# Kernel tuning notes

Measured on AMD Instinct MI355X. Metric: run time of the kernel, lower is better.

## Reference

```python
import jax, jax.numpy as jnp
import numpy as np

EMBED = 1024
HEADS = 16
HEAD_DIM = EMBED // HEADS
BATCH = 4
SEQ = 2048


def setup_inputs() -> dict:
    key = jax.random.key(0)
    ks = jax.random.split(key, 9)
    s = 1.0 / np.sqrt(EMBED)
    inp = {
        "x": jax.random.normal(ks[0], (BATCH, SEQ, EMBED), dtype=jnp.float32),
        "Wq": jax.random.normal(ks[1], (EMBED, EMBED), dtype=jnp.float32) * s,
        "bq": jnp.zeros((EMBED,), jnp.float32),
        "Wk": jax.random.normal(ks[2], (EMBED, EMBED), dtype=jnp.float32) * s,
        "bk": jnp.zeros((EMBED,), jnp.float32),
        "Wv": jax.random.normal(ks[3], (EMBED, EMBED), dtype=jnp.float32) * s,
        "bv": jnp.zeros((EMBED,), jnp.float32),
        "Wo": jax.random.normal(ks[4], (EMBED, EMBED), dtype=jnp.float32) * s,
        "bo": jnp.zeros((EMBED,), jnp.float32),
    }
    return inp


def reference(x, Wq, bq, Wk, bk, Wv, bv, Wo, bo):
    B, S, E = x.shape
    H, D = HEADS, HEAD_DIM
    # projections (torch Linear with weight stored as [in,out] here)
    q = (x @ Wq + bq).reshape(B, S, H, D).transpose(0, 2, 1, 3)  # [B,H,S,D]
    k = (x @ Wk + bk).reshape(B, S, H, D).transpose(0, 2, 1, 3)
    v = (x @ Wv + bv).reshape(B, S, H, D).transpose(0, 2, 1, 3)
    scores = jnp.einsum('bhqd,bhkd->bhqk', q, k) * (1.0 / np.sqrt(D))
    causal = jnp.tril(jnp.ones((S, S), dtype=bool))
    scores = jnp.where(causal[None, None], scores, -jnp.inf)
    attn = jax.nn.softmax(scores, axis=-1)  # dropout p=0.0 -> identity
    out = jnp.einsum('bhqk,bhkd->bhqd', attn, v)  # [B,H,S,D]
    out = out.transpose(0, 2, 1, 3).reshape(B, S, E)
    return out @ Wo + bo
```

## Files before the change

### kernel.cpp

```cpp
#include <hip/hip_runtime.h>
#include <stdint.h>

#define EMBED 1024
#define SEQ   2048
#define BATCH 4
#define HEADS 16
#define HDIM  64
#define LDP   72

typedef unsigned short ushort_t;
typedef __bf16 bf16x8 __attribute__((ext_vector_type(8)));
typedef __bf16 bf16x4 __attribute__((ext_vector_type(4)));
typedef float  f32x4  __attribute__((ext_vector_type(4)));
typedef float  f32x16 __attribute__((ext_vector_type(16)));

#define MFMA16 __builtin_amdgcn_mfma_f32_16x16x32_bf16
#define MFMA32 __builtin_amdgcn_mfma_f32_32x32x16_bf16

typedef __attribute__((address_space(3))) uint32_t lds_u32_t;
typedef __attribute__((address_space(1))) const uint32_t glb_u32_t;

__device__ __forceinline__ void gl_lds16(const ushort_t* g, ushort_t* l) {
    __builtin_amdgcn_global_load_lds((glb_u32_t*)g, (lds_u32_t*)l, 16, 0, 0);
}

__device__ __forceinline__ ushort_t f2bf(float f) {
    union { float f; uint32_t u; } c; c.f = f;
    uint32_t u = c.u;
    return (ushort_t)((u + 0x7FFFu + ((u >> 16) & 1u)) >> 16);
}

__device__ __forceinline__ float exp2f_fast(float x) {
    float r; asm("v_exp_f32 %0, %1" : "=v"(r) : "v"(x)); return r;
}

__global__ __launch_bounds__(256)
void cast_x(const float* __restrict__ X, ushort_t* __restrict__ Xb)
{
    size_t i = ((size_t)blockIdx.x * 256 + threadIdx.x) * 8;
    ushort_t tmp[8];
    #pragma unroll
    for (int e = 0; e < 8; ++e) tmp[e] = f2bf(X[i + e]);
    *(uint4*)(Xb + i) = *(const uint4*)tmp;
}

__global__ __launch_bounds__(256)
void cast_transpose_w(const float* __restrict__ W, ushort_t* __restrict__ Wt)
{
    __shared__ ushort_t Ts[64 * 80];
    const int t = threadIdx.x;
    const int k0 = blockIdx.x * 64, n0 = blockIdx.y * 64;
    const int r = t >> 2, cs = (t & 3) * 16;
    const float* src = W + (size_t)(k0 + r) * EMBED + n0 + cs;
    #pragma unroll
    for (int e = 0; e < 16; ++e) Ts[(cs + e) * 80 + r] = f2bf(src[e]);
    __syncthreads();
    const int n = t >> 2, ks = (t & 3) * 16;
    ushort_t* dst = Wt + (size_t)(n0 + n) * EMBED + k0 + ks;
    *(uint4*)(dst)     = *(const uint4*)(&Ts[n * 80 + ks]);
    *(uint4*)(dst + 8) = *(const uint4*)(&Ts[n * 80 + ks + 8]);
}

__global__ __launch_bounds__(256)
void gemm_qkv(const ushort_t* __restrict__ A, const ushort_t* __restrict__ Bt,
              const float* __restrict__ bq, const float* __restrict__ bk,
              const float* __restrict__ bv, ushort_t* __restrict__ Cq, size_t tsz)
{
    __shared__ ushort_t As[128 * 32];
    __shared__ ushort_t Bs[128 * 32];
    const int t = threadIdx.x;
    const int wave = t >> 6, lane = t & 63;
    const int l15 = lane & 15, quad = lane >> 4;
    const int m0 = blockIdx.y * 128, n0 = blockIdx.x * 128;
    const int wm = (wave >> 1) * 64, wn = (wave & 1) * 64;
    f32x4 acc[4][4] = {};

    const int srow = wave * 32 + (lane >> 2), scol = (lane & 3) * 8;
    const ushort_t* Ag = A  + (size_t)(m0 + srow) * EMBED + scol;
    const ushort_t* Bg = Bt + (size_t)(n0 + srow) * EMBED + scol;
    ushort_t* AsW = As + wave * 1024;
    ushort_t* BsW = Bs + wave * 1024;

    for (int k0 = 0; k0 < EMBED; k0 += 32) {
        gl_lds16(Ag + k0,              AsW);
        gl_lds16(Ag + k0 + 16 * EMBED, AsW + 512);
        gl_lds16(Bg + k0,              BsW);
        gl_lds16(Bg + k0 + 16 * EMBED, BsW + 512);
        __syncthreads();

        bf16x8 af[4], bfr[4];
        #pragma unroll
        for (int mt = 0; mt < 4; ++mt)
            af[mt] = *(const bf16x8*)(&As[(wm + mt * 16 + l15) * 32 + quad * 8]);
        #pragma unroll
        for (int nt = 0; nt < 4; ++nt)
            bfr[nt] = *(const bf16x8*)(&Bs[(wn + nt * 16 + l15) * 32 + quad * 8]);
        #pragma unroll
        for (int mt = 0; mt < 4; ++mt)
            #pragma unroll
            for (int nt = 0; nt < 4; ++nt)
                acc[mt][nt] = MFMA16(af[mt], bfr[nt], acc[mt][nt], 0, 0, 0);
        __syncthreads();
    }

    const int mat = blockIdx.x >> 3;
    const float* bias = (mat == 0) ? bq : (mat == 1) ? bk : bv;
    const float scale = (mat == 0) ? 0.18033688011112042f : 1.0f;
    ushort_t* C = Cq + (size_t)mat * tsz;
    const int nc0 = (blockIdx.x & 7) * 128;
    #pragma unroll
    for (int nt = 0; nt < 4; ++nt) {
        int col = nc0 + wn + nt * 16 + l15;
        float bb = bias[col];
        #pragma unroll
        for (int mt = 0; mt < 4; ++mt)
            #pragma unroll
            for (int r = 0; r < 4; ++r) {
                int row = m0 + wm + mt * 16 + quad * 4 + r;
                C[(size_t)row * EMBED + col] = f2bf((acc[mt][nt][r] + bb) * scale);
            }
    }
}

__global__ __launch_bounds__(256)
void gemm_o(const ushort_t* __restrict__ A, const ushort_t* __restrict__ Bt,
            const float* __restrict__ bias, float* __restrict__ C)
{
    __shared__ ushort_t As[128 * 32];
    __shared__ ushort_t Bs[128 * 32];
    const int t = threadIdx.x;
    const int wave = t >> 6, lane = t & 63;
    const int l15 = lane & 15, quad = lane >> 4;
    const int m0 = blockIdx.y * 128, n0 = blockIdx.x * 128;
    const int wm = (wave >> 1) * 64, wn = (wave & 1) * 64;
    f32x4 acc[4][4] = {};

    const int srow = wave * 32 + (lane >> 2), scol = (lane & 3) * 8;
    const ushort_t* Ag = A  + (size_t)(m0 + srow) * EMBED + scol;
    const ushort_t* Bg = Bt + (size_t)(n0 + srow) * EMBED + scol;
    ushort_t* AsW = As + wave * 1024;
    ushort_t* BsW = Bs + wave * 1024;

    for (int k0 = 0; k0 < EMBED; k0 += 32) {
        gl_lds16(Ag + k0,              AsW);
        gl_lds16(Ag + k0 + 16 * EMBED, AsW + 512);
        gl_lds16(Bg + k0,              BsW);
        gl_lds16(Bg + k0 + 16 * EMBED, BsW + 512);
        __syncthreads();

        bf16x8 af[4], bfr[4];
        #pragma unroll
        for (int mt = 0; mt < 4; ++mt)
            af[mt] = *(const bf16x8*)(&As[(wm + mt * 16 + l15) * 32 + quad * 8]);
        #pragma unroll
        for (int nt = 0; nt < 4; ++nt)
            bfr[nt] = *(const bf16x8*)(&Bs[(wn + nt * 16 + l15) * 32 + quad * 8]);
        #pragma unroll
        for (int mt = 0; mt < 4; ++mt)
            #pragma unroll
            for (int nt = 0; nt < 4; ++nt)
                acc[mt][nt] = MFMA16(af[mt], bfr[nt], acc[mt][nt], 0, 0, 0);
        __syncthreads();
    }

    #pragma unroll
    for (int nt = 0; nt < 4; ++nt) {
        int col = n0 + wn + nt * 16 + l15;
        float bb = bias[col];
        #pragma unroll
        for (int mt = 0; mt < 4; ++mt)
            #pragma unroll
            for (int r = 0; r < 4; ++r) {
                int row = m0 + wm + mt * 16 + quad * 4 + r;
                C[(size_t)row * EMBED + col] = acc[mt][nt][r] + bb;
            }
    }
}

__global__ __launch_bounds__(256)
void transpose_v(const ushort_t* __restrict__ V, ushort_t* __restrict__ Vt)
{
    int blk = blockIdx.x;
    int st = blk & 31, bh = blk >> 5;
    int h = bh & 15, b = bh >> 4;
    int s0 = st * 64;
    __shared__ ushort_t Ts[64 * LDP];
    int tid = threadIdx.x;
    int r = tid >> 2, g = (tid & 3) * 8;

    const ushort_t* src = V + ((size_t)(b * SEQ + s0 + r)) * EMBED + h * HDIM;
    uint4 v0 = *(const uint4*)(src + g);
    uint4 v1 = *(const uint4*)(src + g + 32);
    const ushort_t* e0 = (const ushort_t*)&v0;
    const ushort_t* e1 = (const ushort_t*)&v1;
    #pragma unroll
    for (int e = 0; e < 8; ++e) Ts[(g + e) * LDP + r] = e0[e];
    #pragma unroll
    for (int e = 0; e < 8; ++e) Ts[(g + 32 + e) * LDP + r] = e1[e];
    __syncthreads();

    int d = tid >> 2;
    ushort_t* dst = Vt + ((size_t)bh * HDIM + d) * SEQ + s0;
    *(uint4*)(dst + g)      = *(const uint4*)(&Ts[d * LDP + g]);
    *(uint4*)(dst + g + 32) = *(const uint4*)(&Ts[d * LDP + g + 32]);
}

__global__ __launch_bounds__(256)
void flash_attn(const ushort_t* __restrict__ Q, const ushort_t* __restrict__ K,
                const ushort_t* __restrict__ Vt, ushort_t* __restrict__ O)
{
    const int logical = (blockIdx.x & 7) * 128 + (blockIdx.x >> 3);
    const int bh = logical >> 4;
    const int pb = 15 - (logical & 15);
    const int h = bh & 15, b = bh >> 4;
    const int t = threadIdx.x, w = t >> 6, lane = t & 63;
    const int l31 = lane & 31, hi = lane >> 5;
    const int s = pb * 4 + w;
    const int sdiag = s >> 1;
    const int lastJt = 2 * pb + 1;
    const size_t qkbase = (size_t)b * SEQ * EMBED + (size_t)h * HDIM;
    const size_t vtbase = (size_t)bh * HDIM * SEQ;

    __shared__ ushort_t KsB[2][64 * 64];
    __shared__ ushort_t VsB[2][64 * 64];
    __shared__ float Ls[4][32];

    bf16x8 qb[4];
    const ushort_t* qrow = Q + qkbase + (size_t)(s * 32 + l31) * EMBED + hi * 8;
    #pragma unroll
    for (int ks = 0; ks < 4; ++ks)
        qb[ks] = *(const bf16x8*)(qrow + ks * 16);

    const int rr = lane >> 3, cc = lane & 7;
    const ushort_t* KgL = K  + qkbase + (size_t)(w * 16 + rr) * EMBED + ((cc ^ rr) * 8);
    const ushort_t* VgL = Vt + vtbase + (size_t)(w * 16 + rr) * SEQ  + ((cc ^ rr) * 8);

    f32x16 o0 = {}, o1 = {};
    float l_part = 0.f;

    {
        ushort_t* kd = &KsB[0][w * 1024];
        ushort_t* vd = &VsB[0][w * 1024];
        gl_lds16(KgL,             kd);
        gl_lds16(KgL + 8 * EMBED, kd + 512);
        gl_lds16(VgL,             vd);
        gl_lds16(VgL + 8 * SEQ,   vd + 512);
    }

    int cur = 0;
    for (int jt = 0; jt <= lastJt; ++jt) {
        __syncthreads();

        if (jt < lastJt) {
            const ushort_t* kg = KgL + (size_t)(jt + 1) * 64 * EMBED;
            const ushort_t* vg = VgL + (jt + 1) * 64;
            ushort_t* kd = &KsB[cur ^ 1][w * 1024];
            ushort_t* vd = &VsB[cur ^ 1][w * 1024];
            gl_lds16(kg,             kd);
            gl_lds16(kg + 8 * EMBED, kd + 512);
            gl_lds16(vg,             vd);
            gl_lds16(vg + 8 * SEQ,   vd + 512);
        }

        if (jt <= sdiag) {
            const ushort_t* Kst = &KsB[cur][0];
            const ushort_t* Vst = &VsB[cur][0];
            const bool dg = (jt == sdiag);
            const bool skip1 = dg && !(s & 1);
            const bool mask0 = dg && !(s & 1);
            const bool mask1 = dg && (s & 1);
            const int swz = l31 & 7;

            f32x16 st0 = {}, st1 = {};
            #pragma unroll
            for (int ks = 0; ks < 4; ++ks) {
                bf16x8 ka = *(const bf16x8*)(Kst + l31 * 64 + (((ks * 2 + hi) ^ swz) * 8));
                st0 = MFMA32(ka, qb[ks], st0, 0, 0, 0);
            }
            if (!skip1) {
                #pragma unroll
                for (int ks = 0; ks < 4; ++ks) {
                    bf16x8 ka = *(const bf16x8*)(Kst + (32 + l31) * 64 + (((ks * 2 + hi) ^ swz) * 8));
                    st1 = MFMA32(ka, qb[ks], st1, 0, 0, 0);
                }
            }

            bf16x8 pa0 = {}, pa1 = {}, pa2 = {}, pa3 = {};
            {
                float p[16];
                #pragma unroll
                for (int r = 0; r < 16; ++r) {
                    float pv = exp2f_fast(st0[r]);
                    int key = (r & 3) + 8 * (r >> 2) + 4 * hi;
                    pv = (mask0 && key > l31) ? 0.f : pv;
                    p[r] = pv; l_part += pv;
                }
                #pragma unroll
                for (int e = 0; e < 8; ++e) { pa0[e] = (__bf16)p[e]; pa1[e] = (__bf16)p[8 + e]; }
            }
            if (!skip1) {
                float p[16];
                #pragma unroll
                for (int r = 0; r < 16; ++r) {
                    float pv = exp2f_fast(st1[r]);
                    int key = (r & 3) + 8 * (r >> 2) + 4 * hi;
                    pv = (mask1 && key > l31) ? 0.f : pv;
                    p[r] = pv; l_part += pv;
                }
                #pragma unroll
                for (int e = 0; e < 8; ++e) { pa2[e] = (__bf16)p[e]; pa3[e] = (__bf16)p[8 + e]; }
            }

            #pragma unroll
            for (int ksl = 0; ksl < 4; ++ksl) {
                if (!(ksl >= 2 && skip1)) {
                    bf16x8 pf = (ksl == 0) ? pa0 : (ksl == 1) ? pa1 : (ksl == 2) ? pa2 : pa3;
                    const int c0 = (((ksl * 2)     ^ swz) * 8) + hi * 4;
                    const int c1 = (((ksl * 2 + 1) ^ swz) * 8) + hi * 4;
                    union { bf16x4 hh[2]; bf16x8 v; } u0, u1;
                    u0.hh[0] = *(const bf16x4*)(Vst + l31 * 64 + c0);
                    u0.hh[1] = *(const bf16x4*)(Vst + l31 * 64 + c1);
                    u1.hh[0] = *(const bf16x4*)(Vst + (32 + l31) * 64 + c0);
                    u1.hh[1] = *(const bf16x4*)(Vst + (32 + l31) * 64 + c1);
                    o0 = MFMA32(pf, u0.v, o0, 0, 0, 0);
                    o1 = MFMA32(pf, u1.v, o1, 0, 0, 0);
                }
            }
        }
        cur ^= 1;
    }

    float ltot = l_part + __shfl_xor(l_part, 32);

    if (!hi) Ls[w][l31] = ltot;

    #pragma unroll
    for (int r = 0; r < 16; ++r) {
        int q = (r & 3) + 8 * (r >> 2) + 4 * hi;
        float linv = 1.0f / Ls[w][q];
        size_t ob = qkbase + (size_t)(s * 32 + q) * EMBED;
        O[ob + l31]      = f2bf(o0[r] * linv);
        O[ob + 32 + l31] = f2bf(o1[r] * linv);
    }
}

extern "C" void kernel_launch(void* const* d_in, const int* in_sizes, int n_in,
                              void* d_out, int out_size, void* d_ws, size_t ws_size,
                              hipStream_t stream)
{
    (void)in_sizes; (void)n_in; (void)out_size; (void)ws_size;
    const float* x  = (const float*)d_in[0];
    const float* Wq = (const float*)d_in[1];
    const float* bq = (const float*)d_in[2];
    const float* Wk = (const float*)d_in[3];
    const float* bk = (const float*)d_in[4];
    const float* Wv = (const float*)d_in[5];
    const float* bv = (const float*)d_in[6];
    const float* Wo = (const float*)d_in[7];
    const float* bo = (const float*)d_in[8];
    float* out = (float*)d_out;

    const int M = BATCH * SEQ;
    size_t tsz = (size_t)M * EMBED;
    size_t wsz = (size_t)EMBED * EMBED;
    ushort_t* xb  = (ushort_t*)d_ws;
    ushort_t* Qb  = xb + tsz;
    ushort_t* Kb  = Qb + tsz;
    ushort_t* Vb  = Kb + tsz;
    ushort_t* Vt  = Vb + tsz;
    ushort_t* Wt0 = Vt + tsz;
    ushort_t* Wt1 = Wt0 + wsz;
    ushort_t* Wt2 = Wt1 + wsz;
    ushort_t* Wt3 = Wt2 + wsz;
    ushort_t* Ob  = xb;

    dim3 wg(16, 16);
    cast_x<<<4096, 256, 0, stream>>>(x, xb);
    cast_transpose_w<<<wg, 256, 0, stream>>>(Wq, Wt0);
    cast_transpose_w<<<wg, 256, 0, stream>>>(Wk, Wt1);
    cast_transpose_w<<<wg, 256, 0, stream>>>(Wv, Wt2);
    cast_transpose_w<<<wg, 256, 0, stream>>>(Wo, Wt3);

    gemm_qkv<<<dim3(24, 64), 256, 0, stream>>>(xb, Wt0, bq, bk, bv, Qb, tsz);

    transpose_v<<<BATCH * HEADS * (SEQ / 64), 256, 0, stream>>>(Vb, Vt);
    flash_attn<<<BATCH * HEADS * (SEQ / 128), 256, 0, stream>>>(Qb, Kb, Vt, Ob);

    gemm_o<<<dim3(8, 64), 256, 0, stream>>>(Ob, Wt3, bo, out);
}
```

Before: 285.6 us.

## Pair mirrored causal query strips per wave to balance work and share K/V tiles

Each wave now handles two query strips, s and 63-s, so every block carries the same causal workload. K and V tiles loaded into LDS are reused for both strips, and the grid is halved to 512 blocks. The row-sum is now accumulated by an MFMA against a ones vector rather than with scalar adds, which also removes the LDS reduction. In exchange, register pressure roughly doubles (four output accumulators, two l accumulators, two Q fragments), which may lower occupancy.

```diff
diff --git a/kernel.cpp b/kernel.cpp
--- a/kernel.cpp
+++ b/kernel.cpp
@@ -209,34 +209,44 @@
 void flash_attn(const ushort_t* __restrict__ Q, const ushort_t* __restrict__ K,
                 const ushort_t* __restrict__ Vt, ushort_t* __restrict__ O)
 {
-    const int logical = (blockIdx.x & 7) * 128 + (blockIdx.x >> 3);
-    const int bh = logical >> 4;
-    const int pb = 15 - (logical & 15);
+    const int logical = (blockIdx.x & 7) * 64 + (blockIdx.x >> 3);
+    const int bh = logical >> 3;
+    const int p  = logical & 7;
     const int h = bh & 15, b = bh >> 4;
     const int t = threadIdx.x, w = t >> 6, lane = t & 63;
     const int l31 = lane & 31, hi = lane >> 5;
-    const int s = pb * 4 + w;
-    const int sdiag = s >> 1;
-    const int lastJt = 2 * pb + 1;
+    const int sA = 4 * p + w, sB = 63 - sA;
+    const int dA = sA >> 1, dB = sB >> 1;
+    const int oddA = sA & 1, oddB = sB & 1;
+    const int lastJt = (63 - 4 * p) >> 1;
     const size_t qkbase = (size_t)b * SEQ * EMBED + (size_t)h * HDIM;
     const size_t vtbase = (size_t)bh * HDIM * SEQ;
 
     __shared__ ushort_t KsB[2][64 * 64];
     __shared__ ushort_t VsB[2][64 * 64];
-    __shared__ float Ls[4][32];
-
-    bf16x8 qb[4];
-    const ushort_t* qrow = Q + qkbase + (size_t)(s * 32 + l31) * EMBED + hi * 8;
-    #pragma unroll
-    for (int ks = 0; ks < 4; ++ks)
-        qb[ks] = *(const bf16x8*)(qrow + ks * 16);
+
+    bf16x8 qbA[4], qbB[4];
+    {
+        const ushort_t* qrA = Q + qkbase + (size_t)(sA * 32 + l31) * EMBED + hi * 8;
+        const ushort_t* qrB = Q + qkbase + (size_t)(sB * 32 + l31) * EMBED + hi * 8;
+        #pragma unroll
+        for (int ks = 0; ks < 4; ++ks) {
+            qbA[ks] = *(const bf16x8*)(qrA + ks * 16);
+            qbB[ks] = *(const bf16x8*)(qrB + ks * 16);
+        }
+    }
+
+    union { uint32_t u[4]; bf16x8 v; } onesu;
+    onesu.u[0] = onesu.u[1] = onesu.u[2] = onesu.u[3] = 0x3F803F80u;
+    const bf16x8 ones = onesu.v;
 
     const int rr = lane >> 3, cc = lane & 7;
     const ushort_t* KgL = K  + qkbase + (size_t)(w * 16 + rr) * EMBED + ((cc ^ rr) * 8);
     const ushort_t* VgL = Vt + vtbase + (size_t)(w * 16 + rr) * SEQ  + ((cc ^ rr) * 8);
 
-    f32x16 o0 = {}, o1 = {};
-    float l_part = 0.f;
+    f32x16 oA0 = {}, oA1 = {}, oB0 = {}, oB1 = {};
+    f32x16 lA = {}, lB = {};
+    const int swz = l31 & 7;
 
     {
         ushort_t* kd = &KsB[0][w * 1024];
@@ -247,8 +257,8 @@
         gl_lds16(VgL + 8 * SEQ,   vd + 512);
     }
 
-    int cur = 0;
     for (int jt = 0; jt <= lastJt; ++jt) {
+        const int cur = jt & 1;
         __syncthreads();
 
         if (jt < lastJt) {
@@ -262,85 +272,122 @@
             gl_lds16(vg + 8 * SEQ,   vd + 512);
         }
 
-        if (jt <= sdiag) {
-            const ushort_t* Kst = &KsB[cur][0];
-            const ushort_t* Vst = &VsB[cur][0];
-            const bool dg = (jt == sdiag);
-            const bool skip1 = dg && !(s & 1);
-            const bool mask0 = dg && !(s & 1);
-            const bool mask1 = dg && (s & 1);
-            const int swz = l31 & 7;
-
-            f32x16 st0 = {}, st1 = {};
+        if (jt > dB) continue;
+        const ushort_t* Kst = &KsB[cur][0];
+        const ushort_t* Vst = &VsB[cur][0];
+        const bool aA  = (jt <= dA);
+        const bool dgA = (jt == dA), dgB = (jt == dB);
+        const bool haveA1 = aA && !(dgA && !oddA);
+        const bool haveB1 = !(dgB && !oddB);
+
+        f32x16 stA0 = {}, stA1 = {}, stB0 = {}, stB1 = {};
+        #pragma unroll
+        for (int ks = 0; ks < 4; ++ks) {
+            bf16x8 k0 = *(const bf16x8*)(Kst + l31 * 64 + (((ks * 2 + hi) ^ swz) * 8));
+            stB0 = MFMA32(k0, qbB[ks], stB0, 0, 0, 0);
+            if (aA) stA0 = MFMA32(k0, qbA[ks], stA0, 0, 0, 0);
+        }
+        if (haveB1 || haveA1) {
             #pragma unroll
             for (int ks = 0; ks < 4; ++ks) {
-                bf16x8 ka = *(const bf16x8*)(Kst + l31 * 64 + (((ks * 2 + hi) ^ swz) * 8));
-                st0 = MFMA32(ka, qb[ks], st0, 0, 0, 0);
-            }
-            if (!skip1) {
-                #pragma unroll
-                for (int ks = 0; ks < 4; ++ks) {
-                    bf16x8 ka = *(const bf16x8*)(Kst + (32 + l31) * 64 + (((ks * 2 + hi) ^ swz) * 8));
-                    st1 = MFMA32(ka, qb[ks], st1, 0, 0, 0);
+                bf16x8 k1 = *(const bf16x8*)(Kst + (32 + l31) * 64 + (((ks * 2 + hi) ^ swz) * 8));
+                if (haveB1) stB1 = MFMA32(k1, qbB[ks], stB1, 0, 0, 0);
+                if (haveA1) stA1 = MFMA32(k1, qbA[ks], stA1, 0, 0, 0);
+            }
+        }
+
+        bf16x8 pA0 = {}, pA1 = {}, pA2 = {}, pA3 = {};
+        bf16x8 pB0 = {}, pB1 = {}, pB2 = {}, pB3 = {};
+        {
+            float p0[16];
+            #pragma unroll
+            for (int r = 0; r < 16; ++r) p0[r] = exp2f_fast(stB0[r]);
+            if (dgB && !oddB) {
+                #pragma unroll
+                for (int r = 0; r < 16; ++r) {
+                    int key = (r & 3) + 8 * (r >> 2) + 4 * hi;
+                    if (key > l31) p0[r] = 0.f;
                 }
             }
-
-            bf16x8 pa0 = {}, pa1 = {}, pa2 = {}, pa3 = {};
-            {
-                float p[16];
+            #pragma unroll
+            for (int e = 0; e < 8; ++e) { pB0[e] = (__bf16)p0[e]; pB1[e] = (__bf16)p0[8 + e]; }
+            if (haveB1) {
+                float p1[16];
+                #pragma unroll
+                for (int r = 0; r < 16; ++r) p1[r] = exp2f_fast(stB1[r]);
+                if (dgB && oddB) {
+                    #pragma unroll
+                    for (int r = 0; r < 16; ++r) {
+                        int key = (r & 3) + 8 * (r >> 2) + 4 * hi;
+                        if (key > l31) p1[r] = 0.f;
+                    }
+                }
+                #pragma unroll
+                for (int e = 0; e < 8; ++e) { pB2[e] = (__bf16)p1[e]; pB3[e] = (__bf16)p1[8 + e]; }
+            }
+        }
+        if (aA) {
+            float p0[16];
+            #pragma unroll
+            for (int r = 0; r < 16; ++r) p0[r] = exp2f_fast(stA0[r]);
+            if (dgA && !oddA) {
                 #pragma unroll
                 for (int r = 0; r < 16; ++r) {
-                    float pv = exp2f_fast(st0[r]);
                     int key = (r & 3) + 8 * (r >> 2) + 4 * hi;
-                    pv = (mask0 && key > l31) ? 0.f : pv;
-                    p[r] = pv; l_part += pv;
+                    if (key > l31) p0[r] = 0.f;
                 }
-                #pragma unroll
-                for (int e = 0; e < 8; ++e) { pa0[e] = (__bf16)p[e]; pa1[e] = (__bf16)p[8 + e]; }
-            }
-            if (!skip1) {
-                float p[16];
-                #pragma unroll
-                for (int r = 0; r < 16; ++r) {
-                    float pv = exp2f_fast(st1[r]);
-                    int key = (r & 3) + 8 * (r >> 2) + 4 * hi;
-                    pv = (mask1 && key > l31) ? 0.f : pv;
-                    p[r] = pv; l_part += pv;
+            }
+            #pragma unroll
+            for (int e = 0; e < 8; ++e) { pA0[e] = (__bf16)p0[e]; pA1[e] = (__bf16)p0[8 + e]; }
+            if (haveA1) {
+                float p1[16];
+                #pragma unroll
+                for (int r = 0; r < 16; ++r) p1[r] = exp2f_fast(stA1[r]);
+                if (dgA && oddA) {
+                    #pragma unroll
+                    for (int r = 0; r < 16; ++r) {
+                        int key = (r & 3) + 8 * (r >> 2) + 4 * hi;
+                        if (key > l31) p1[r] = 0.f;
+                    }
                 }
                 #pragma unroll
-                for (int e = 0; e < 8; ++e) { pa2[e] = (__bf16)p[e]; pa3[e] = (__bf16)p[8 + e]; }
-            }
-
-            #pragma unroll
-            for (int ksl = 0; ksl < 4; ++ksl) {
-                if (!(ksl >= 2 && skip1)) {
-                    bf16x8 pf = (ksl == 0) ? pa0 : (ksl == 1) ? pa1 : (ksl == 2) ? pa2 : pa3;
-                    const int c0 = (((ksl * 2)     ^ swz) * 8) + hi * 4;
-                    const int c1 = (((ksl * 2 + 1) ^ swz) * 8) + hi * 4;
-                    union { bf16x4 hh[2]; bf16x8 v; } u0, u1;
-                    u0.hh[0] = *(const bf16x4*)(Vst + l31 * 64 + c0);
-                    u0.hh[1] = *(const bf16x4*)(Vst + l31 * 64 + c1);
-                    u1.hh[0] = *(const bf16x4*)(Vst + (32 + l31) * 64 + c0);
-                    u1.hh[1] = *(const bf16x4*)(Vst + (32 + l31) * 64 + c1);
-                    o0 = MFMA32(pf, u0.v, o0, 0, 0, 0);
-                    o1 = MFMA32(pf, u1.v, o1, 0, 0, 0);
-                }
-            }
-        }
-        cur ^= 1;
-    }
-
-    float ltot = l_part + __shfl_xor(l_part, 32);
-
-    if (!hi) Ls[w][l31] = ltot;
+                for (int e = 0; e < 8; ++e) { pA2[e] = (__bf16)p1[e]; pA3[e] = (__bf16)p1[8 + e]; }
+            }
+        }
+
+        #pragma unroll
+        for (int ksl = 0; ksl < 4; ++ksl) {
+            const int c0 = (((ksl * 2)     ^ swz) * 8) + hi * 4;
+            const int c1 = (((ksl * 2 + 1) ^ swz) * 8) + hi * 4;
+            union { bf16x4 hh[2]; bf16x8 v; } u0, u1;
+            u0.hh[0] = *(const bf16x4*)(Vst + l31 * 64 + c0);
+            u0.hh[1] = *(const bf16x4*)(Vst + l31 * 64 + c1);
+            u1.hh[0] = *(const bf16x4*)(Vst + (32 + l31) * 64 + c0);
+            u1.hh[1] = *(const bf16x4*)(Vst + (32 + l31) * 64 + c1);
+            bf16x8 pB = (ksl == 0) ? pB0 : (ksl == 1) ? pB1 : (ksl == 2) ? pB2 : pB3;
+            oB0 = MFMA32(pB, u0.v, oB0, 0, 0, 0);
+            oB1 = MFMA32(pB, u1.v, oB1, 0, 0, 0);
+            lB  = MFMA32(pB, ones, lB, 0, 0, 0);
+            if (aA) {
+                bf16x8 pA = (ksl == 0) ? pA0 : (ksl == 1) ? pA1 : (ksl == 2) ? pA2 : pA3;
+                oA0 = MFMA32(pA, u0.v, oA0, 0, 0, 0);
+                oA1 = MFMA32(pA, u1.v, oA1, 0, 0, 0);
+                lA  = MFMA32(pA, ones, lA, 0, 0, 0);
+            }
+        }
+    }
 
     #pragma unroll
     for (int r = 0; r < 16; ++r) {
         int q = (r & 3) + 8 * (r >> 2) + 4 * hi;
-        float linv = 1.0f / Ls[w][q];
-        size_t ob = qkbase + (size_t)(s * 32 + q) * EMBED;
-        O[ob + l31]      = f2bf(o0[r] * linv);
-        O[ob + 32 + l31] = f2bf(o1[r] * linv);
+        float invA = 1.0f / lA[r];
+        float invB = 1.0f / lB[r];
+        size_t obA = qkbase + (size_t)(sA * 32 + q) * EMBED;
+        size_t obB = qkbase + (size_t)(sB * 32 + q) * EMBED;
+        O[obA + l31]      = f2bf(oA0[r] * invA);
+        O[obA + 32 + l31] = f2bf(oA1[r] * invA);
+        O[obB + l31]      = f2bf(oB0[r] * invB);
+        O[obB + 32 + l31] = f2bf(oB1[r] * invB);
     }
 }
 
@@ -384,7 +431,7 @@
     gemm_qkv<<<dim3(24, 64), 256, 0, stream>>>(xb, Wt0, bq, bk, bv, Qb, tsz);
 
     transpose_v<<<BATCH * HEADS * (SEQ / 64), 256, 0, stream>>>(Vb, Vt);
-    flash_attn<<<BATCH * HEADS * (SEQ / 128), 256, 0, stream>>>(Qb, Kb, Vt, Ob);
+    flash_attn<<<512, 256, 0, stream>>>(Qb, Kb, Vt, Ob);
 
     gemm_o<<<dim3(8, 64), 256, 0, stream>>>(Ob, Wt3, bo, out);
 }
```

After: 328.4 us. 1.15x slower.

## Split attention key range across two wave halves and merge partials via LDS

Applied to the files above, without the earlier changes.

Each flash-attention block now runs 512 threads. Two groups of four waves each process half of the key tiles for the same query rows, then combine their partial outputs and row sums through shared memory. The softmax denominator is now accumulated with an extra MFMA against a ones vector instead of scalar adds and shuffles. Block-to-XCD mapping is reworked so each XCD keeps whole heads. This shortens the serial key loop per block to improve latency and balance. The cost is extra MFMA work, a final LDS reduction with two barriers, and higher per-block register and LDS pressure.

```diff
diff --git a/kernel.cpp b/kernel.cpp
--- a/kernel.cpp
+++ b/kernel.cpp
@@ -205,110 +205,118 @@
     *(uint4*)(dst + g + 32) = *(const uint4*)(&Ts[d * LDP + g + 32]);
 }
 
-__global__ __launch_bounds__(256)
+__global__ __launch_bounds__(512, 4)
 void flash_attn(const ushort_t* __restrict__ Q, const ushort_t* __restrict__ K,
                 const ushort_t* __restrict__ Vt, ushort_t* __restrict__ O)
 {
-    const int logical = (blockIdx.x & 7) * 128 + (blockIdx.x >> 3);
-    const int bh = logical >> 4;
-    const int pb = 15 - (logical & 15);
+    const int xcd = blockIdx.x & 7, c = blockIdx.x >> 3;
+    const int p  = 15 - (c >> 3);
+    const int bh = xcd * 8 + (c & 7);
     const int h = bh & 15, b = bh >> 4;
     const int t = threadIdx.x, w = t >> 6, lane = t & 63;
+    const int wl = w & 3, hf = w >> 2;
     const int l31 = lane & 31, hi = lane >> 5;
-    const int s = pb * 4 + w;
+    const int s = 4 * p + wl;
     const int sdiag = s >> 1;
-    const int lastJt = 2 * pb + 1;
+    const int odd = s & 1;
+    const int R = p + 1;
+    const int jt0 = hf ? (p + 1) : 0;
     const size_t qkbase = (size_t)b * SEQ * EMBED + (size_t)h * HDIM;
     const size_t vtbase = (size_t)bh * HDIM * SEQ;
 
-    __shared__ ushort_t KsB[2][64 * 64];
-    __shared__ ushort_t VsB[2][64 * 64];
-    __shared__ float Ls[4][32];
+    __shared__ __attribute__((aligned(16))) ushort_t smem[32768];
 
     bf16x8 qb[4];
-    const ushort_t* qrow = Q + qkbase + (size_t)(s * 32 + l31) * EMBED + hi * 8;
-    #pragma unroll
-    for (int ks = 0; ks < 4; ++ks)
-        qb[ks] = *(const bf16x8*)(qrow + ks * 16);
+    {
+        const ushort_t* qrow = Q + qkbase + (size_t)(s * 32 + l31) * EMBED + hi * 8;
+        #pragma unroll
+        for (int ks = 0; ks < 4; ++ks) qb[ks] = *(const bf16x8*)(qrow + ks * 16);
+    }
+
+    union { uint32_t u[4]; bf16x8 v; } onesu;
+    onesu.u[0] = onesu.u[1] = onesu.u[2] = onesu.u[3] = 0x3F803F80u;
+    const bf16x8 ones = onesu.v;
 
     const int rr = lane >> 3, cc = lane & 7;
-    const ushort_t* KgL = K  + qkbase + (size_t)(w * 16 + rr) * EMBED + ((cc ^ rr) * 8);
-    const ushort_t* VgL = Vt + vtbase + (size_t)(w * 16 + rr) * SEQ  + ((cc ^ rr) * 8);
-
-    f32x16 o0 = {}, o1 = {};
-    float l_part = 0.f;
+    const ushort_t* Kg = K  + qkbase + (size_t)(jt0 * 64 + wl * 16 + rr) * EMBED + ((cc ^ rr) * 8);
+    const ushort_t* Vg = Vt + vtbase + (size_t)(wl * 16 + rr) * SEQ + jt0 * 64 + ((cc ^ rr) * 8);
+
+    f32x16 o0 = {}, o1 = {}, lac = {};
+    const int swz = l31 & 7;
 
     {
-        ushort_t* kd = &KsB[0][w * 1024];
-        ushort_t* vd = &VsB[0][w * 1024];
-        gl_lds16(KgL,             kd);
-        gl_lds16(KgL + 8 * EMBED, kd + 512);
-        gl_lds16(VgL,             vd);
-        gl_lds16(VgL + 8 * SEQ,   vd + 512);
-    }
-
-    int cur = 0;
-    for (int jt = 0; jt <= lastJt; ++jt) {
+        ushort_t* kd = smem + (hf * 2 + 0) * 4096 + wl * 1024;
+        ushort_t* vd = smem + 16384 + (hf * 2 + 0) * 4096 + wl * 1024;
+        gl_lds16(Kg,             kd);
+        gl_lds16(Kg + 8 * EMBED, kd + 512);
+        gl_lds16(Vg,             vd);
+        gl_lds16(Vg + 8 * SEQ,   vd + 512);
+    }
+
+    for (int r = 0; r < R; ++r) {
+        const int cur = r & 1;
         __syncthreads();
 
-        if (jt < lastJt) {
-            const ushort_t* kg = KgL + (size_t)(jt + 1) * 64 * EMBED;
-            const ushort_t* vg = VgL + (jt + 1) * 64;
-            ushort_t* kd = &KsB[cur ^ 1][w * 1024];
-            ushort_t* vd = &VsB[cur ^ 1][w * 1024];
+        if (r + 1 < R) {
+            const ushort_t* kg = Kg + (size_t)(r + 1) * 64 * EMBED;
+            const ushort_t* vg = Vg + (r + 1) * 64;
+            ushort_t* kd = smem + (hf * 2 + (cur ^ 1)) * 4096 + wl * 1024;
+            ushort_t* vd = smem + 16384 + (hf * 2 + (cur ^ 1)) * 4096 + wl * 1024;
             gl_lds16(kg,             kd);
             gl_lds16(kg + 8 * EMBED, kd + 512);
             gl_lds16(vg,             vd);
             gl_lds16(vg + 8 * SEQ,   vd + 512);
         }
 
+        const int jt = jt0 + r;
         if (jt <= sdiag) {
-            const ushort_t* Kst = &KsB[cur][0];
-            const ushort_t* Vst = &VsB[cur][0];
+            const ushort_t* Kst = smem + (hf * 2 + cur) * 4096;
+            const ushort_t* Vst = smem + 16384 + (hf * 2 + cur) * 4096;
             const bool dg = (jt == sdiag);
-            const bool skip1 = dg && !(s & 1);
-            const bool mask0 = dg && !(s & 1);
-            const bool mask1 = dg && (s & 1);
-            const int swz = l31 & 7;
+            const bool skip1 = dg && !odd;
 
             f32x16 st0 = {}, st1 = {};
             #pragma unroll
             for (int ks = 0; ks < 4; ++ks) {
-                bf16x8 ka = *(const bf16x8*)(Kst + l31 * 64 + (((ks * 2 + hi) ^ swz) * 8));
-                st0 = MFMA32(ka, qb[ks], st0, 0, 0, 0);
+                bf16x8 k0 = *(const bf16x8*)(Kst + l31 * 64 + (((ks * 2 + hi) ^ swz) * 8));
+                st0 = MFMA32(k0, qb[ks], st0, 0, 0, 0);
             }
             if (!skip1) {
                 #pragma unroll
                 for (int ks = 0; ks < 4; ++ks) {
-                    bf16x8 ka = *(const bf16x8*)(Kst + (32 + l31) * 64 + (((ks * 2 + hi) ^ swz) * 8));
-                    st1 = MFMA32(ka, qb[ks], st1, 0, 0, 0);
+                    bf16x8 k1 = *(const bf16x8*)(Kst + (32 + l31) * 64 + (((ks * 2 + hi) ^ swz) * 8));
+                    st1 = MFMA32(k1, qb[ks], st1, 0, 0, 0);
                 }
             }
 
             bf16x8 pa0 = {}, pa1 = {}, pa2 = {}, pa3 = {};
             {
-                float p[16];
+                float p0[16];
                 #pragma unroll
-                for (int r = 0; r < 16; ++r) {
-                    float pv = exp2f_fast(st0[r]);
-                    int key = (r & 3) + 8 * (r >> 2) + 4 * hi;
-                    pv = (mask0 && key > l31) ? 0.f : pv;
-                    p[r] = pv; l_part += pv;
+                for (int r2 = 0; r2 < 16; ++r2) p0[r2] = exp2f_fast(st0[r2]);
+                if (dg && !odd) {
+                    #pragma unroll
+                    for (int r2 = 0; r2 < 16; ++r2) {
+                        int key = (r2 & 3) + 8 * (r2 >> 2) + 4 * hi;
+                        if (key > l31) p0[r2] = 0.f;
+                    }
                 }
                 #pragma unroll
-                for (int e = 0; e < 8; ++e) { pa0[e] = (__bf16)p[e]; pa1[e] = (__bf16)p[8 + e]; }
-            }
-            if (!skip1) {
-                float p[16];
-                #pragma unroll
-                for (int r = 0; r < 16; ++r) {
-                    float pv = exp2f_fast(st1[r]);
-                    int key = (r & 3) + 8 * (r >> 2) + 4 * hi;
-                    pv = (mask1 && key > l31) ? 0.f : pv;
-                    p[r] = pv; l_part += pv;
+                for (int e = 0; e < 8; ++e) { pa0[e] = (__bf16)p0[e]; pa1[e] = (__bf16)p0[8 + e]; }
+                if (!skip1) {
+                    float p1[16];
+                    #pragma unroll
+                    for (int r2 = 0; r2 < 16; ++r2) p1[r2] = exp2f_fast(st1[r2]);
+                    if (dg && odd) {
+                        #pragma unroll
+                        for (int r2 = 0; r2 < 16; ++r2) {
+                            int key = (r2 & 3) + 8 * (r2 >> 2) + 4 * hi;
+                            if (key > l31) p1[r2] = 0.f;
+                        }
+                    }
+                    #pragma unroll
+                    for (int e = 0; e < 8; ++e) { pa2[e] = (__bf16)p1[e]; pa3[e] = (__bf16)p1[8 + e]; }
                 }
-                #pragma unroll
-                for (int e = 0; e < 8; ++e) { pa2[e] = (__bf16)p[e]; pa3[e] = (__bf16)p[8 + e]; }
             }
 
             #pragma unroll
@@ -322,25 +330,39 @@
                     u0.hh[1] = *(const bf16x4*)(Vst + l31 * 64 + c1);
                     u1.hh[0] = *(const bf16x4*)(Vst + (32 + l31) * 64 + c0);
                     u1.hh[1] = *(const bf16x4*)(Vst + (32 + l31) * 64 + c1);
-                    o0 = MFMA32(pf, u0.v, o0, 0, 0, 0);
-                    o1 = MFMA32(pf, u1.v, o1, 0, 0, 0);
+                    o0  = MFMA32(pf, u0.v, o0, 0, 0, 0);
+                    o1  = MFMA32(pf, u1.v, o1, 0, 0, 0);
+                    lac = MFMA32(pf, ones, lac, 0, 0, 0);
                 }
             }
         }
-        cur ^= 1;
-    }
-
-    float ltot = l_part + __shfl_xor(l_part, 32);
-
-    if (!hi) Ls[w][l31] = ltot;
-
-    #pragma unroll
-    for (int r = 0; r < 16; ++r) {
-        int q = (r & 3) + 8 * (r >> 2) + 4 * hi;
-        float linv = 1.0f / Ls[w][q];
-        size_t ob = qkbase + (size_t)(s * 32 + q) * EMBED;
-        O[ob + l31]      = f2bf(o0[r] * linv);
-        O[ob + 32 + l31] = f2bf(o1[r] * linv);
+    }
+
+    __syncthreads();
+    float* Cs = (float*)smem;
+    if (hf) {
+        float* dst = Cs + (wl * 64 + lane) * 49;
+        #pragma unroll
+        for (int r2 = 0; r2 < 16; ++r2) {
+            dst[r2]      = o0[r2];
+            dst[16 + r2] = o1[r2];
+            dst[32 + r2] = lac[r2];
+        }
+    }
+    __syncthreads();
+    if (!hf) {
+        const float* src = Cs + (wl * 64 + lane) * 49;
+        #pragma unroll
+        for (int r2 = 0; r2 < 16; ++r2) {
+            float t0 = o0[r2]  + src[r2];
+            float t1 = o1[r2]  + src[16 + r2];
+            float lt = lac[r2] + src[32 + r2];
+            float inv = 1.0f / lt;
+            int q = (r2 & 3) + 8 * (r2 >> 2) + 4 * hi;
+            size_t ob = qkbase + (size_t)(s * 32 + q) * EMBED;
+            O[ob + l31]      = f2bf(t0 * inv);
+            O[ob + 32 + l31] = f2bf(t1 * inv);
+        }
     }
 }
 
@@ -384,7 +406,7 @@
     gemm_qkv<<<dim3(24, 64), 256, 0, stream>>>(xb, Wt0, bq, bk, bv, Qb, tsz);
 
     transpose_v<<<BATCH * HEADS * (SEQ / 64), 256, 0, stream>>>(Vb, Vt);
-    flash_attn<<<BATCH * HEADS * (SEQ / 128), 256, 0, stream>>>(Qb, Kb, Vt, Ob);
+    flash_attn<<<1024, 512, 0, stream>>>(Qb, Kb, Vt, Ob);
 
     gemm_o<<<dim3(8, 64), 256, 0, stream>>>(Ob, Wt3, bo, out);
 }
```

Measured after the change: 271.2 us. -5.0%, faster.
